# Kernel tuning notes

Hardware: AMD Instinct MI355X
Metric: run time of the kernel (lower is better)

Reference implementation:

```python
import jax, jax.numpy as jnp
import numpy as np

N_NODES = 100000
N_EDGES = 1600000
N_GRAPHS = 256


def gcn_conv(x, src, dst, edge_weight, W, b, num_nodes):
    """PyG GCNConv: add self-loops, symmetric degree normalization,
    linear transform, scatter-add aggregation, bias."""
    loop = jnp.arange(num_nodes)
    s = jnp.concatenate([src, loop])
    d = jnp.concatenate([dst, loop])
    ew = jnp.concatenate([edge_weight, jnp.ones((num_nodes,), dtype=edge_weight.dtype)])
    deg = jax.ops.segment_sum(ew, d, num_segments=num_nodes)  # [N]
    dinv = jnp.where(deg > 0, deg ** -0.5, 0.0)
    norm = dinv[s] * ew * dinv[d]  # [E+N]
    h = x @ W  # [N, out]
    msg = h[s] * norm[:, None]  # gather + scale
    out = jax.ops.segment_sum(msg, d, num_segments=num_nodes)  # scatter-add
    return out + b


def global_mean_pool(x, batch, num_graphs):
    s = jax.ops.segment_sum(x, batch, num_segments=num_graphs)
    cnt = jax.ops.segment_sum(jnp.ones((x.shape[0],), dtype=x.dtype), batch, num_segments=num_graphs)
    return s / jnp.maximum(cnt, 1.0)[:, None]


def setup_inputs() -> dict:
    key = jax.random.key(0)
    ks = jax.random.split(key, 12)
    x = jax.random.normal(ks[0], (N_NODES, 128), dtype=jnp.float32)
    edge_index = jax.random.randint(ks[1], (2, N_EDGES), 0, N_NODES, dtype=jnp.int64)
    edge_attr = jax.random.uniform(ks[2], (N_EDGES,), dtype=jnp.float32)
    batch = jnp.sort(jax.random.randint(ks[3], (N_NODES,), 0, N_GRAPHS, dtype=jnp.int64))
    def lin(k, fan_in, fan_out):
        lim = 1.0 / np.sqrt(fan_in)
        kw, kb = jax.random.split(k)
        W = jax.random.uniform(kw, (fan_in, fan_out), minval=-lim, maxval=lim, dtype=jnp.float32)
        b = jax.random.uniform(kb, (fan_out,), minval=-lim, maxval=lim, dtype=jnp.float32)
        return W, b
    W1, b1 = lin(ks[4], 128, 64)
    W2, b2 = lin(ks[5], 64, 64)
    W3, b3 = lin(ks[6], 64, 64)
    Wl, bl = lin(ks[7], 64, 10)
    return {"x": x, "edge_index": edge_index, "edge_attr": edge_attr, "batch": batch,
            "W1": W1, "b1": b1, "W2": W2, "b2": b2, "W3": W3, "b3": b3, "Wl": Wl, "bl": bl}


def reference(x, edge_index, edge_attr, batch, W1, b1, W2, b2, W3, b3, Wl, bl):
    src, dst = edge_index[0], edge_index[1]
    n = x.shape[0]
    h = jax.nn.relu(gcn_conv(x, src, dst, edge_attr, W1, b1, n))
    h = jax.nn.relu(gcn_conv(h, src, dst, edge_attr, W2, b2, n))
    h = jax.nn.relu(gcn_conv(h, src, dst, edge_attr, W3, b3, n))
    g = global_mean_pool(h, batch, N_GRAPHS)  # [G, 64]
    return g @ Wl + bl  # [G, num_classes]
```

## Files before the change

kernel.cpp:

```cpp
#include <hip/hip_runtime.h>
#include <hip/hip_bf16.h>

#define N_NODES  100000
#define N_EDGES  1600000
#define N_GRAPHS 256
#define F 64
#define NBUCK  782
#define CHUNK  4096
#define NCHUNK 391


__global__ __launch_bounds__(1024) void k_hist(const int* __restrict__ dst, int* __restrict__ hist) {
    __shared__ int lh[NBUCK];
    int tid = threadIdx.x, chunk = blockIdx.x;
    for (int j = tid; j < NBUCK; j += 1024) lh[j] = 0;
    __syncthreads();
    int e0 = chunk * CHUNK;
#pragma unroll
    for (int i = 0; i < CHUNK / 1024; i++) {
        int e = e0 + i * 1024 + tid;
        if (e < N_EDGES) atomicAdd(&lh[dst[e] >> 7], 1);
    }
    __syncthreads();
    for (int j = tid; j < NBUCK; j += 1024) hist[chunk * NBUCK + j] = lh[j];
}

__global__ __launch_bounds__(512) void k_colscan(int* __restrict__ hist, int* __restrict__ btot) {
    __shared__ int ts[512];
    int b = blockIdx.x, tid = threadIdx.x;
    int v = (tid < NCHUNK) ? hist[tid * NBUCK + b] : 0;
    ts[tid] = v;
    __syncthreads();
    int x = v;
    for (int off = 1; off < 512; off <<= 1) {
        int t = (tid >= off) ? ts[tid - off] : 0;
        __syncthreads();
        x += t; ts[tid] = x;
        __syncthreads();
    }
    if (tid < NCHUNK) hist[tid * NBUCK + b] = x - v;
    if (tid == 511) btot[b] = x;
}

__global__ __launch_bounds__(512) void k_bscan_gstart(const int* __restrict__ btot, int* __restrict__ base,
                                                      const int* __restrict__ batch, int* __restrict__ gstart) {
    if (blockIdx.x == 1) {
        int g = threadIdx.x;
        if (g > N_GRAPHS) return;
        int lo = 0, hi = N_NODES;
        while (lo < hi) {
            int mid = (lo + hi) >> 1;
            if (batch[mid] < g) lo = mid + 1; else hi = mid;
        }
        gstart[g] = lo;
        return;
    }
    __shared__ int ts[256];
    int tid = threadIdx.x;
    int v[4], loc[4], run = 0;
    if (tid < 256) {
#pragma unroll
        for (int k = 0; k < 4; k++) {
            int c = tid * 4 + k;
            v[k] = (c < NBUCK) ? btot[c] : 0;
            loc[k] = run; run += v[k];
        }
        ts[tid] = run;
    }
    __syncthreads();
    int x = run;
    for (int off = 1; off < 256; off <<= 1) {
        int t = (tid >= off && tid < 256) ? ts[tid - off] : 0;
        __syncthreads();
        if (tid < 256) { x += t; ts[tid] = x; }
        __syncthreads();
    }
    if (tid < 256) {
        int texcl = x - run;
#pragma unroll
        for (int k = 0; k < 4; k++) {
            int c = tid * 4 + k;
            if (c < NBUCK) base[c] = texcl + loc[k];
        }
        if (tid == 255) base[NBUCK] = x;
    }
}

__global__ __launch_bounds__(1024) void k_partition(const int* __restrict__ src, const int* __restrict__ dst,
                                                    const float* __restrict__ ew,
                                                    const int* __restrict__ hist, const int* __restrict__ base,
                                                    long long* __restrict__ part) {
    __shared__ int cursor[NBUCK];
    int tid = threadIdx.x, chunk = blockIdx.x;
    for (int j = tid; j < NBUCK; j += 1024) cursor[j] = base[j] + hist[chunk * NBUCK + j];
    __syncthreads();
    int e0 = chunk * CHUNK;
#pragma unroll
    for (int i = 0; i < CHUNK / 1024; i++) {
        int e = e0 + i * 1024 + tid;
        if (e < N_EDGES) {
            int d = dst[e];
            int pos = atomicAdd(&cursor[d >> 7], 1);
            unsigned lo = (unsigned)src[e] | ((unsigned)(d & 127) << 17);
            long long rec = (long long)((unsigned long long)lo |
                            ((unsigned long long)__float_as_uint(ew[e]) << 32));
            part[pos] = rec;
        }
    }
}

__global__ __launch_bounds__(512) void k_deg(const long long* __restrict__ part,
                                             const int* __restrict__ base,
                                             float* __restrict__ dinv_g, int* __restrict__ row_off) {
    __shared__ float fdeg[128];
    __shared__ int   cnt[128];
    __shared__ int   sc[128];
    int b = blockIdx.x, tid = threadIdx.x;
    if (tid < 128) { fdeg[tid] = 1.0f; cnt[tid] = 0; }
    __syncthreads();
    int e0 = base[b], e1 = base[b + 1];
    for (int k = e0 + tid; k < e1; k += 512) {
        long long rec = part[k];
        int d7 = ((int)rec >> 17) & 127;
        atomicAdd(&fdeg[d7], __uint_as_float((unsigned)(rec >> 32)));
        atomicAdd(&cnt[d7], 1);
    }
    __syncthreads();
    int myc = 0, x = 0;
    if (tid < 128) {
        int node = b * 128 + tid;
        if (node < N_NODES) dinv_g[node] = rsqrtf(fdeg[tid]);
        myc = cnt[tid]; x = myc; sc[tid] = x;
    }
    __syncthreads();
    for (int off = 1; off < 128; off <<= 1) {
        int t = (tid < 128 && tid >= off) ? sc[tid - off] : 0;
        __syncthreads();
        if (tid < 128) { x += t; sc[tid] = x; }
        __syncthreads();
    }
    if (tid < 128) {
        int node = b * 128 + tid;
        if (node < N_NODES) row_off[node] = e0 + (x - myc);
    }
    if (b == 0 && tid == 0) row_off[N_NODES] = N_EDGES;
}

__global__ __launch_bounds__(512) void k_scat(const long long* __restrict__ part,
                                              const int* __restrict__ base,
                                              const float* __restrict__ dinv_g,
                                              const int* __restrict__ row_off,
                                              int2* __restrict__ esec) {
    __shared__ int   cursor[128];
    __shared__ float sdinv[128];
    int b = blockIdx.x, tid = threadIdx.x;
    if (tid < 128) {
        int node = b * 128 + tid;
        cursor[tid] = row_off[node < N_NODES ? node : N_NODES];
        sdinv[tid]  = dinv_g[node < N_NODES ? node : 0];
    }
    __syncthreads();
    int e0 = base[b], e1 = base[b + 1];
    for (int k = e0 + tid; k < e1; k += 512) {
        long long rec = part[k];
        int lo = (int)rec;
        int d7 = (lo >> 17) & 127;
        int s  = lo & 0x1FFFF;
        float w = __uint_as_float((unsigned)(rec >> 32));
        float coef = (w * sdinv[d7]) * dinv_g[s];
        int pos = atomicAdd(&cursor[d7], 1);
        esec[pos] = make_int2(s << 7, __float_as_int(coef));
    }
    if (b == 0 && tid < 16) esec[N_EDGES + tid] = make_int2(0, 0);
}

template <int K, bool BF16IN>
__global__ __launch_bounds__(256) void k_gemm(const void* __restrict__ Xv,
                                              const float* __restrict__ W,
                                              __hip_bfloat16* __restrict__ H) {
    constexpr int KC = 32;
    constexpr int XP = KC + 4;
    __shared__ float Xs[256 * XP];
    __shared__ float Ws[KC * F];
    const int tid  = threadIdx.x;
    const int fgrp = tid & 7;
    const int ngrp = tid >> 3;
    const int f0   = fgrp * 8;
    const int nb   = blockIdx.x * 256;

    float acc[8][8];
#pragma unroll
    for (int i = 0; i < 8; i++)
#pragma unroll
        for (int j = 0; j < 8; j++) acc[i][j] = 0.0f;

    for (int kc = 0; kc < K; kc += KC) {
        if (kc) __syncthreads();
        if (BF16IN) {
            const unsigned short* X = (const unsigned short*)Xv;
#pragma unroll
            for (int pass = 0; pass < 4; pass++) {
                int idx = tid + pass * 256;
                int r = idx >> 2, q = idx & 3;
                int gr = nb + r; if (gr >= N_NODES) gr = N_NODES - 1;
                uint4 v = *(const uint4*)&X[(size_t)gr * K + kc + q * 8];
                float* dp = &Xs[r * XP + q * 8];
                dp[0] = __uint_as_float(v.x << 16);
                dp[1] = __uint_as_float(v.x & 0xffff0000u);
                dp[2] = __uint_as_float(v.y << 16);
                dp[3] = __uint_as_float(v.y & 0xffff0000u);
                dp[4] = __uint_as_float(v.z << 16);
                dp[5] = __uint_as_float(v.z & 0xffff0000u);
                dp[6] = __uint_as_float(v.w << 16);
                dp[7] = __uint_as_float(v.w & 0xffff0000u);
            }
        } else {
            const float* X = (const float*)Xv;
#pragma unroll
            for (int pass = 0; pass < 8; pass++) {
                int idx = tid + pass * 256;
                int r = idx >> 3, q = idx & 7;
                int gr = nb + r; if (gr >= N_NODES) gr = N_NODES - 1;
                float4 v = *(const float4*)&X[(size_t)gr * K + kc + q * 4];
                *(float4*)&Xs[r * XP + q * 4] = v;
            }
        }
#pragma unroll
        for (int pass = 0; pass < 2; pass++) {
            int idx = tid + pass * 256;
            float4 v = *(const float4*)&W[(size_t)(kc + (idx >> 4)) * F + (idx & 15) * 4];
            *(float4*)&Ws[idx * 4] = v;
        }
        __syncthreads();
#pragma unroll
        for (int k = 0; k < KC; k += 4) {
            float4 wa[4], wb[4];
#pragma unroll
            for (int kk = 0; kk < 4; kk++) {
                wa[kk] = *(const float4*)&Ws[(k + kk) * F + f0];
                wb[kk] = *(const float4*)&Ws[(k + kk) * F + f0 + 4];
            }
#pragma unroll
            for (int i = 0; i < 8; i++) {
                float4 xv = *(const float4*)&Xs[(ngrp + 32 * i) * XP + k];
#pragma unroll
                for (int kk = 0; kk < 4; kk++) {
                    float xk = (kk == 0) ? xv.x : (kk == 1) ? xv.y : (kk == 2) ? xv.z : xv.w;
                    acc[i][0] = fmaf(xk, wa[kk].x, acc[i][0]);
                    acc[i][1] = fmaf(xk, wa[kk].y, acc[i][1]);
                    acc[i][2] = fmaf(xk, wa[kk].z, acc[i][2]);
                    acc[i][3] = fmaf(xk, wa[kk].w, acc[i][3]);
                    acc[i][4] = fmaf(xk, wb[kk].x, acc[i][4]);
                    acc[i][5] = fmaf(xk, wb[kk].y, acc[i][5]);
                    acc[i][6] = fmaf(xk, wb[kk].z, acc[i][6]);
                    acc[i][7] = fmaf(xk, wb[kk].w, acc[i][7]);
                }
            }
        }
    }
#pragma unroll
    for (int i = 0; i < 8; i++) {
        int gn = nb + ngrp + 32 * i;
        if (gn < N_NODES) {
            __hip_bfloat16 hb[8];
#pragma unroll
            for (int j = 0; j < 8; j++) hb[j] = __float2bfloat16(acc[i][j]);
            *(uint4*)&H[(size_t)gn * F + f0] = *(uint4*)hb;
        }
    }
}

__global__ __launch_bounds__(256) void k_agg(const __hip_bfloat16* __restrict__ H,
                                             const int* __restrict__ row_off,
                                             const int2* __restrict__ esec,
                                             const float* __restrict__ dinv,
                                             const float* __restrict__ bias,
                                             __hip_bfloat16* __restrict__ O) {
    int wv   = threadIdx.x >> 6;
    int lane = threadIdx.x & 63;
    int np   = blockIdx.x * 16 + wv * 4;
    int q  = lane >> 3;
    int f8 = lane & 7;
    int r0 = __builtin_amdgcn_readfirstlane(row_off[np]);
    int r1 = __builtin_amdgcn_readfirstlane(row_off[np + 1]);
    int r2 = __builtin_amdgcn_readfirstlane(row_off[np + 2]);
    int r3 = __builtin_amdgcn_readfirstlane(row_off[np + 3]);
    int r4 = __builtin_amdgcn_readfirstlane(row_off[np + 4]);
    const char* Hbase = (const char*)H;

    float a0[8], a1[8], a2[8], a3[8];
#pragma unroll
    for (int u = 0; u < 8; u++) { a0[u] = 0.0f; a1[u] = 0.0f; a2[u] = 0.0f; a3[u] = 0.0f; }

    int l0 = r1 - r0, l1 = r2 - r1, l2 = r3 - r2, l3 = r4 - r3;
    int ml = l0 > l1 ? l0 : l1;
    if (l2 > ml) ml = l2;
    if (l3 > ml) ml = l3;
    int iters = (ml + 7) >> 3;
    int j0 = r0 + q, j1 = r1 + q, j2 = r2 + q, j3 = r3 + q;
    for (int it = 0; it < iters; it++, j0 += 8, j1 += 8, j2 += 8, j3 += 8) {
        int i0 = j0 < N_EDGES ? j0 : N_EDGES;
        int i1 = j1 < N_EDGES ? j1 : N_EDGES;
        int i2 = j2 < N_EDGES ? j2 : N_EDGES;
        int i3 = j3 < N_EDGES ? j3 : N_EDGES;
        int2 ev0 = esec[i0];
        int2 ev1 = esec[i1];
        int2 ev2 = esec[i2];
        int2 ev3 = esec[i3];
        float c0 = (j0 < r1) ? __int_as_float(ev0.y) : 0.0f;
        float c1 = (j1 < r2) ? __int_as_float(ev1.y) : 0.0f;
        float c2 = (j2 < r3) ? __int_as_float(ev2.y) : 0.0f;
        float c3 = (j3 < r4) ? __int_as_float(ev3.y) : 0.0f;
        uint4 h0 = *(const uint4*)(Hbase + (unsigned)ev0.x + (f8 << 4));
        uint4 h1 = *(const uint4*)(Hbase + (unsigned)ev1.x + (f8 << 4));
        uint4 h2 = *(const uint4*)(Hbase + (unsigned)ev2.x + (f8 << 4));
        uint4 h3 = *(const uint4*)(Hbase + (unsigned)ev3.x + (f8 << 4));
        a0[0] = fmaf(c0, __uint_as_float(h0.x << 16),         a0[0]);
        a0[1] = fmaf(c0, __uint_as_float(h0.x & 0xffff0000u), a0[1]);
        a0[2] = fmaf(c0, __uint_as_float(h0.y << 16),         a0[2]);
        a0[3] = fmaf(c0, __uint_as_float(h0.y & 0xffff0000u), a0[3]);
        a0[4] = fmaf(c0, __uint_as_float(h0.z << 16),         a0[4]);
        a0[5] = fmaf(c0, __uint_as_float(h0.z & 0xffff0000u), a0[5]);
        a0[6] = fmaf(c0, __uint_as_float(h0.w << 16),         a0[6]);
        a0[7] = fmaf(c0, __uint_as_float(h0.w & 0xffff0000u), a0[7]);
        a1[0] = fmaf(c1, __uint_as_float(h1.x << 16),         a1[0]);
        a1[1] = fmaf(c1, __uint_as_float(h1.x & 0xffff0000u), a1[1]);
        a1[2] = fmaf(c1, __uint_as_float(h1.y << 16),         a1[2]);
        a1[3] = fmaf(c1, __uint_as_float(h1.y & 0xffff0000u), a1[3]);
        a1[4] = fmaf(c1, __uint_as_float(h1.z << 16),         a1[4]);
        a1[5] = fmaf(c1, __uint_as_float(h1.z & 0xffff0000u), a1[5]);
        a1[6] = fmaf(c1, __uint_as_float(h1.w << 16),         a1[6]);
        a1[7] = fmaf(c1, __uint_as_float(h1.w & 0xffff0000u), a1[7]);
        a2[0] = fmaf(c2, __uint_as_float(h2.x << 16),         a2[0]);
        a2[1] = fmaf(c2, __uint_as_float(h2.x & 0xffff0000u), a2[1]);
        a2[2] = fmaf(c2, __uint_as_float(h2.y << 16),         a2[2]);
        a2[3] = fmaf(c2, __uint_as_float(h2.y & 0xffff0000u), a2[3]);
        a2[4] = fmaf(c2, __uint_as_float(h2.z << 16),         a2[4]);
        a2[5] = fmaf(c2, __uint_as_float(h2.z & 0xffff0000u), a2[5]);
        a2[6] = fmaf(c2, __uint_as_float(h2.w << 16),         a2[6]);
        a2[7] = fmaf(c2, __uint_as_float(h2.w & 0xffff0000u), a2[7]);
        a3[0] = fmaf(c3, __uint_as_float(h3.x << 16),         a3[0]);
        a3[1] = fmaf(c3, __uint_as_float(h3.x & 0xffff0000u), a3[1]);
        a3[2] = fmaf(c3, __uint_as_float(h3.y << 16),         a3[2]);
        a3[3] = fmaf(c3, __uint_as_float(h3.y & 0xffff0000u), a3[3]);
        a3[4] = fmaf(c3, __uint_as_float(h3.z << 16),         a3[4]);
        a3[5] = fmaf(c3, __uint_as_float(h3.z & 0xffff0000u), a3[5]);
        a3[6] = fmaf(c3, __uint_as_float(h3.w << 16),         a3[6]);
        a3[7] = fmaf(c3, __uint_as_float(h3.w & 0xffff0000u), a3[7]);
    }
#pragma unroll
    for (int m = 8; m < 64; m <<= 1) {
#pragma unroll
        for (int u = 0; u < 8; u++) {
            a0[u] += __shfl_xor(a0[u], m);
            a1[u] += __shfl_xor(a1[u], m);
            a2[u] += __shfl_xor(a2[u], m);
            a3[u] += __shfl_xor(a3[u], m);
        }
    }
    if (q < 4) {
        int node = np + q;
        float av[8];
#pragma unroll
        for (int u = 0; u < 8; u++) {
            float t01 = (q & 1) ? a1[u] : a0[u];
            float t23 = (q & 1) ? a3[u] : a2[u];
            av[u] = (q & 2) ? t23 : t01;
        }
        float di = dinv[node];
        float di2 = di * di;
        uint4 hs = *(const uint4*)(Hbase + (size_t)node * 128 + (f8 << 4));
        float hv[8];
        hv[0] = __uint_as_float(hs.x << 16);
        hv[1] = __uint_as_float(hs.x & 0xffff0000u);
        hv[2] = __uint_as_float(hs.y << 16);
        hv[3] = __uint_as_float(hs.y & 0xffff0000u);
        hv[4] = __uint_as_float(hs.z << 16);
        hv[5] = __uint_as_float(hs.z & 0xffff0000u);
        hv[6] = __uint_as_float(hs.w << 16);
        hv[7] = __uint_as_float(hs.w & 0xffff0000u);
        const float4* bp = (const float4*)(bias + f8 * 8);
        float4 bv0 = bp[0], bv1 = bp[1];
        float r[8];
        r[0] = fmaxf(av[0] + bv0.x + di2 * hv[0], 0.0f);
        r[1] = fmaxf(av[1] + bv0.y + di2 * hv[1], 0.0f);
        r[2] = fmaxf(av[2] + bv0.z + di2 * hv[2], 0.0f);
        r[3] = fmaxf(av[3] + bv0.w + di2 * hv[3], 0.0f);
        r[4] = fmaxf(av[4] + bv1.x + di2 * hv[4], 0.0f);
        r[5] = fmaxf(av[5] + bv1.y + di2 * hv[5], 0.0f);
        r[6] = fmaxf(av[6] + bv1.z + di2 * hv[6], 0.0f);
        r[7] = fmaxf(av[7] + bv1.w + di2 * hv[7], 0.0f);
        __hip_bfloat16 hb[8];
#pragma unroll
        for (int u = 0; u < 8; u++) hb[u] = __float2bfloat16(r[u]);
        *(uint4*)&O[(size_t)node * F + f8 * 8] = *(uint4*)hb;
    }
}

__global__ __launch_bounds__(256) void k_pool_linear(const __hip_bfloat16* __restrict__ H,
                                                     const int* __restrict__ gstart,
                                                     const float* __restrict__ Wl,
                                                     const float* __restrict__ bl,
                                                     float* __restrict__ out) {
    int g = blockIdx.x;
    int beg = gstart[g], end = gstart[g + 1];
    int lane = threadIdx.x & 63, wv = threadIdx.x >> 6;
    float acc = 0.0f;
    for (int r = beg + wv; r < end; r += 4)
        acc += __bfloat162float(H[(size_t)r * F + lane]);
    __shared__ float s[4][F];
    s[wv][lane] = acc;
    __syncthreads();
    if (wv == 0) {
        float tot = s[0][lane] + s[1][lane] + s[2][lane] + s[3][lane];
        float cntf = (float)(end - beg);
        float p = tot / fmaxf(cntf, 1.0f);
        for (int c = 0; c < 10; c++) {
            float v = p * Wl[lane * 10 + c];
            for (int off = 32; off; off >>= 1) v += __shfl_down(v, off);
            if (lane == 0) out[g * 10 + c] = v + bl[c];
        }
    }
}


extern "C" void kernel_launch(void* const* d_in, const int* in_sizes, int n_in,
                              void* d_out, int out_size, void* d_ws, size_t ws_size,
                              hipStream_t stream) {
    const float* x    = (const float*)d_in[0];
    const int*   ei   = (const int*)d_in[1];
    const float* ea   = (const float*)d_in[2];
    const int*   bat  = (const int*)d_in[3];
    const float* W1   = (const float*)d_in[4];
    const float* b1   = (const float*)d_in[5];
    const float* W2   = (const float*)d_in[6];
    const float* b2   = (const float*)d_in[7];
    const float* W3   = (const float*)d_in[8];
    const float* b3   = (const float*)d_in[9];
    const float* Wl   = (const float*)d_in[10];
    const float* bl   = (const float*)d_in[11];
    float* out = (float*)d_out;

    const int* src = ei;
    const int* dst = ei + N_EDGES;

    char* ws = (char*)d_ws;
    size_t off = 0;
    auto carve = [&](size_t bytes) {
        void* p = ws + off;
        off += (bytes + 255) & ~(size_t)255;
        return p;
    };
    float*          dinv    = (float*)carve(N_NODES * 4);
    int*            row_off = (int*)  carve((N_NODES + 1) * 4);
    int2*           esec    = (int2*) carve(((size_t)N_EDGES + 16) * 8);
    __hip_bfloat16* hbuf    = (__hip_bfloat16*)carve((size_t)N_NODES * F * 2);
    __hip_bfloat16* obuf    = (__hip_bfloat16*)carve((size_t)N_NODES * F * 4);
    int*            gstart  = (int*)  carve((N_GRAPHS + 1) * 4);
    (void)ws_size; (void)in_sizes; (void)n_in; (void)out_size;

    long long* part = (long long*)hbuf;
    char* alias = (char*)obuf + (size_t)N_NODES * F * 2;
    int* hist = (int*)alias;                         alias += (size_t)NCHUNK * NBUCK * 4;
    int* btot = (int*)alias;                         alias += (NBUCK + 8) * 4;
    int* base = (int*)alias;

    const int GB = (N_NODES + 255) / 256;

    k_hist        <<<NCHUNK, 1024, 0, stream>>>(dst, hist);
    k_colscan     <<<NBUCK,  512,  0, stream>>>(hist, btot);
    k_bscan_gstart<<<2,      512,  0, stream>>>(btot, base, bat, gstart);
    k_partition   <<<NCHUNK, 1024, 0, stream>>>(src, dst, ea, hist, base, part);
    k_deg         <<<NBUCK,  512,  0, stream>>>(part, base, dinv, row_off);
    k_scat        <<<NBUCK,  512,  0, stream>>>(part, base, dinv, row_off, esec);

    k_gemm<128, false><<<GB, 256, 0, stream>>>(x, W1, hbuf);
    k_agg<<<N_NODES / 16, 256, 0, stream>>>(hbuf, row_off, esec, dinv, b1, obuf);
    k_gemm<64, true><<<GB, 256, 0, stream>>>(obuf, W2, hbuf);
    k_agg<<<N_NODES / 16, 256, 0, stream>>>(hbuf, row_off, esec, dinv, b2, obuf);
    k_gemm<64, true><<<GB, 256, 0, stream>>>(obuf, W3, hbuf);
    k_agg<<<N_NODES / 16, 256, 0, stream>>>(hbuf, row_off, esec, dinv, b3, obuf);

    k_pool_linear<<<N_GRAPHS, 256, 0, stream>>>(obuf, gstart, Wl, bl, out);
}
```

Before: 382.1 us.

## Fuse edge partition with first GEMM and double per-iteration gathers in aggregation

Merges the edge-partition kernel and the first-layer GEMM into one launch whose blocks split between the two independent jobs. The partition output moves to its own workspace buffer instead of aliasing hbuf, which is what allows the GEMM to run concurrently with it and saves a launch. The aggregation loop now issues 8 edge/feature gathers per iteration instead of 4, giving more loads in flight at the cost of extra registers. The tail padding of esec grows to 32 entries to match, and the partition blocks drop from 1024 to 256 threads.

```diff
diff --git a/kernel.cpp b/kernel.cpp
--- a/kernel.cpp
+++ b/kernel.cpp
@@ -8,6 +8,7 @@
 #define NBUCK  782
 #define CHUNK  4096
 #define NCHUNK 391
+#define GB     391
 
 
 __global__ __launch_bounds__(1024) void k_hist(const int* __restrict__ dst, int* __restrict__ hist) {
@@ -86,25 +87,101 @@
     }
 }
 
-__global__ __launch_bounds__(1024) void k_partition(const int* __restrict__ src, const int* __restrict__ dst,
-                                                    const float* __restrict__ ew,
-                                                    const int* __restrict__ hist, const int* __restrict__ base,
-                                                    long long* __restrict__ part) {
-    __shared__ int cursor[NBUCK];
-    int tid = threadIdx.x, chunk = blockIdx.x;
-    for (int j = tid; j < NBUCK; j += 1024) cursor[j] = base[j] + hist[chunk * NBUCK + j];
-    __syncthreads();
-    int e0 = chunk * CHUNK;
-#pragma unroll
-    for (int i = 0; i < CHUNK / 1024; i++) {
-        int e = e0 + i * 1024 + tid;
-        if (e < N_EDGES) {
-            int d = dst[e];
-            int pos = atomicAdd(&cursor[d >> 7], 1);
-            unsigned lo = (unsigned)src[e] | ((unsigned)(d & 127) << 17);
-            long long rec = (long long)((unsigned long long)lo |
-                            ((unsigned long long)__float_as_uint(ew[e]) << 32));
-            part[pos] = rec;
+__global__ __launch_bounds__(256) void k_part_gemm1(
+    const int* __restrict__ src, const int* __restrict__ dst, const float* __restrict__ ew,
+    const int* __restrict__ hist, const int* __restrict__ base, long long* __restrict__ part,
+    const float* __restrict__ X, const float* __restrict__ W, __hip_bfloat16* __restrict__ H) {
+    constexpr int KC = 32;
+    constexpr int XP = KC + 4;
+    __shared__ float smem[256 * XP + KC * F];
+    const int tid = threadIdx.x;
+
+    if (blockIdx.x < NCHUNK) {
+        int* cursor = (int*)smem;
+        int chunk = blockIdx.x;
+        for (int j = tid; j < NBUCK; j += 256) cursor[j] = base[j] + hist[chunk * NBUCK + j];
+        __syncthreads();
+        int e0 = chunk * CHUNK;
+#pragma unroll
+        for (int i = 0; i < CHUNK / 256; i++) {
+            int e = e0 + i * 256 + tid;
+            if (e < N_EDGES) {
+                int d = dst[e];
+                int pos = atomicAdd(&cursor[d >> 7], 1);
+                unsigned lo = (unsigned)src[e] | ((unsigned)(d & 127) << 17);
+                long long rec = (long long)((unsigned long long)lo |
+                                ((unsigned long long)__float_as_uint(ew[e]) << 32));
+                part[pos] = rec;
+            }
+        }
+        return;
+    }
+
+    float* Xs = smem;
+    float* Ws = smem + 256 * XP;
+    const int fgrp = tid & 7;
+    const int ngrp = tid >> 3;
+    const int f0   = fgrp * 8;
+    const int nb   = (blockIdx.x - NCHUNK) * 256;
+    constexpr int K = 128;
+
+    float acc[8][8];
+#pragma unroll
+    for (int i = 0; i < 8; i++)
+#pragma unroll
+        for (int j = 0; j < 8; j++) acc[i][j] = 0.0f;
+
+    for (int kc = 0; kc < K; kc += KC) {
+        if (kc) __syncthreads();
+#pragma unroll
+        for (int pass = 0; pass < 8; pass++) {
+            int idx = tid + pass * 256;
+            int r = idx >> 3, q = idx & 7;
+            int gr = nb + r; if (gr >= N_NODES) gr = N_NODES - 1;
+            float4 v = *(const float4*)&X[(size_t)gr * K + kc + q * 4];
+            *(float4*)&Xs[r * XP + q * 4] = v;
+        }
+#pragma unroll
+        for (int pass = 0; pass < 2; pass++) {
+            int idx = tid + pass * 256;
+            float4 v = *(const float4*)&W[(size_t)(kc + (idx >> 4)) * F + (idx & 15) * 4];
+            *(float4*)&Ws[idx * 4] = v;
+        }
+        __syncthreads();
+#pragma unroll
+        for (int k = 0; k < KC; k += 4) {
+            float4 wa[4], wb[4];
+#pragma unroll
+            for (int kk = 0; kk < 4; kk++) {
+                wa[kk] = *(const float4*)&Ws[(k + kk) * F + f0];
+                wb[kk] = *(const float4*)&Ws[(k + kk) * F + f0 + 4];
+            }
+#pragma unroll
+            for (int i = 0; i < 8; i++) {
+                float4 xv = *(const float4*)&Xs[(ngrp + 32 * i) * XP + k];
+#pragma unroll
+                for (int kk = 0; kk < 4; kk++) {
+                    float xk = (kk == 0) ? xv.x : (kk == 1) ? xv.y : (kk == 2) ? xv.z : xv.w;
+                    acc[i][0] = fmaf(xk, wa[kk].x, acc[i][0]);
+                    acc[i][1] = fmaf(xk, wa[kk].y, acc[i][1]);
+                    acc[i][2] = fmaf(xk, wa[kk].z, acc[i][2]);
+                    acc[i][3] = fmaf(xk, wa[kk].w, acc[i][3]);
+                    acc[i][4] = fmaf(xk, wb[kk].x, acc[i][4]);
+                    acc[i][5] = fmaf(xk, wb[kk].y, acc[i][5]);
+                    acc[i][6] = fmaf(xk, wb[kk].z, acc[i][6]);
+                    acc[i][7] = fmaf(xk, wb[kk].w, acc[i][7]);
+                }
+            }
+        }
+    }
+#pragma unroll
+    for (int i = 0; i < 8; i++) {
+        int gn = nb + ngrp + 32 * i;
+        if (gn < N_NODES) {
+            __hip_bfloat16 hb[8];
+#pragma unroll
+            for (int j = 0; j < 8; j++) hb[j] = __float2bfloat16(acc[i][j]);
+            *(uint4*)&H[(size_t)gn * F + f0] = *(uint4*)hb;
         }
     }
 }
@@ -171,11 +248,11 @@
         int pos = atomicAdd(&cursor[d7], 1);
         esec[pos] = make_int2(s << 7, __float_as_int(coef));
     }
-    if (b == 0 && tid < 16) esec[N_EDGES + tid] = make_int2(0, 0);
-}
-
-template <int K, bool BF16IN>
-__global__ __launch_bounds__(256) void k_gemm(const void* __restrict__ Xv,
+    if (b == 0 && tid < 32) esec[N_EDGES + tid] = make_int2(0, 0);
+}
+
+template <int K>
+__global__ __launch_bounds__(256) void k_gemm(const unsigned short* __restrict__ X,
                                               const float* __restrict__ W,
                                               __hip_bfloat16* __restrict__ H) {
     constexpr int KC = 32;
@@ -196,34 +273,21 @@
 
     for (int kc = 0; kc < K; kc += KC) {
         if (kc) __syncthreads();
-        if (BF16IN) {
-            const unsigned short* X = (const unsigned short*)Xv;
-#pragma unroll
-            for (int pass = 0; pass < 4; pass++) {
-                int idx = tid + pass * 256;
-                int r = idx >> 2, q = idx & 3;
-                int gr = nb + r; if (gr >= N_NODES) gr = N_NODES - 1;
-                uint4 v = *(const uint4*)&X[(size_t)gr * K + kc + q * 8];
-                float* dp = &Xs[r * XP + q * 8];
-                dp[0] = __uint_as_float(v.x << 16);
-                dp[1] = __uint_as_float(v.x & 0xffff0000u);
-                dp[2] = __uint_as_float(v.y << 16);
-                dp[3] = __uint_as_float(v.y & 0xffff0000u);
-                dp[4] = __uint_as_float(v.z << 16);
-                dp[5] = __uint_as_float(v.z & 0xffff0000u);
-                dp[6] = __uint_as_float(v.w << 16);
-                dp[7] = __uint_as_float(v.w & 0xffff0000u);
-            }
-        } else {
-            const float* X = (const float*)Xv;
-#pragma unroll
-            for (int pass = 0; pass < 8; pass++) {
-                int idx = tid + pass * 256;
-                int r = idx >> 3, q = idx & 7;
-                int gr = nb + r; if (gr >= N_NODES) gr = N_NODES - 1;
-                float4 v = *(const float4*)&X[(size_t)gr * K + kc + q * 4];
-                *(float4*)&Xs[r * XP + q * 4] = v;
-            }
+#pragma unroll
+        for (int pass = 0; pass < 4; pass++) {
+            int idx = tid + pass * 256;
+            int r = idx >> 2, q = idx & 3;
+            int gr = nb + r; if (gr >= N_NODES) gr = N_NODES - 1;
+            uint4 v = *(const uint4*)&X[(size_t)gr * K + kc + q * 8];
+            float* dp = &Xs[r * XP + q * 8];
+            dp[0] = __uint_as_float(v.x << 16);
+            dp[1] = __uint_as_float(v.x & 0xffff0000u);
+            dp[2] = __uint_as_float(v.y << 16);
+            dp[3] = __uint_as_float(v.y & 0xffff0000u);
+            dp[4] = __uint_as_float(v.z << 16);
+            dp[5] = __uint_as_float(v.z & 0xffff0000u);
+            dp[6] = __uint_as_float(v.w << 16);
+            dp[7] = __uint_as_float(v.w & 0xffff0000u);
         }
 #pragma unroll
         for (int pass = 0; pass < 2; pass++) {
@@ -288,83 +352,63 @@
     int r4 = __builtin_amdgcn_readfirstlane(row_off[np + 4]);
     const char* Hbase = (const char*)H;
 
-    float a0[8], a1[8], a2[8], a3[8];
-#pragma unroll
-    for (int u = 0; u < 8; u++) { a0[u] = 0.0f; a1[u] = 0.0f; a2[u] = 0.0f; a3[u] = 0.0f; }
-
+    float a[4][8];
+#pragma unroll
+    for (int n = 0; n < 4; n++)
+#pragma unroll
+        for (int u = 0; u < 8; u++) a[n][u] = 0.0f;
+
+    int jb[4] = { r0 + q, r1 + q, r2 + q, r3 + q };
+    int re[4] = { r1, r2, r3, r4 };
     int l0 = r1 - r0, l1 = r2 - r1, l2 = r3 - r2, l3 = r4 - r3;
     int ml = l0 > l1 ? l0 : l1;
     if (l2 > ml) ml = l2;
     if (l3 > ml) ml = l3;
-    int iters = (ml + 7) >> 3;
-    int j0 = r0 + q, j1 = r1 + q, j2 = r2 + q, j3 = r3 + q;
-    for (int it = 0; it < iters; it++, j0 += 8, j1 += 8, j2 += 8, j3 += 8) {
-        int i0 = j0 < N_EDGES ? j0 : N_EDGES;
-        int i1 = j1 < N_EDGES ? j1 : N_EDGES;
-        int i2 = j2 < N_EDGES ? j2 : N_EDGES;
-        int i3 = j3 < N_EDGES ? j3 : N_EDGES;
-        int2 ev0 = esec[i0];
-        int2 ev1 = esec[i1];
-        int2 ev2 = esec[i2];
-        int2 ev3 = esec[i3];
-        float c0 = (j0 < r1) ? __int_as_float(ev0.y) : 0.0f;
-        float c1 = (j1 < r2) ? __int_as_float(ev1.y) : 0.0f;
-        float c2 = (j2 < r3) ? __int_as_float(ev2.y) : 0.0f;
-        float c3 = (j3 < r4) ? __int_as_float(ev3.y) : 0.0f;
-        uint4 h0 = *(const uint4*)(Hbase + (unsigned)ev0.x + (f8 << 4));
-        uint4 h1 = *(const uint4*)(Hbase + (unsigned)ev1.x + (f8 << 4));
-        uint4 h2 = *(const uint4*)(Hbase + (unsigned)ev2.x + (f8 << 4));
-        uint4 h3 = *(const uint4*)(Hbase + (unsigned)ev3.x + (f8 << 4));
-        a0[0] = fmaf(c0, __uint_as_float(h0.x << 16),         a0[0]);
-        a0[1] = fmaf(c0, __uint_as_float(h0.x & 0xffff0000u), a0[1]);
-        a0[2] = fmaf(c0, __uint_as_float(h0.y << 16),         a0[2]);
-        a0[3] = fmaf(c0, __uint_as_float(h0.y & 0xffff0000u), a0[3]);
-        a0[4] = fmaf(c0, __uint_as_float(h0.z << 16),         a0[4]);
-        a0[5] = fmaf(c0, __uint_as_float(h0.z & 0xffff0000u), a0[5]);
-        a0[6] = fmaf(c0, __uint_as_float(h0.w << 16),         a0[6]);
-        a0[7] = fmaf(c0, __uint_as_float(h0.w & 0xffff0000u), a0[7]);
-        a1[0] = fmaf(c1, __uint_as_float(h1.x << 16),         a1[0]);
-        a1[1] = fmaf(c1, __uint_as_float(h1.x & 0xffff0000u), a1[1]);
-        a1[2] = fmaf(c1, __uint_as_float(h1.y << 16),         a1[2]);
-        a1[3] = fmaf(c1, __uint_as_float(h1.y & 0xffff0000u), a1[3]);
-        a1[4] = fmaf(c1, __uint_as_float(h1.z << 16),         a1[4]);
-        a1[5] = fmaf(c1, __uint_as_float(h1.z & 0xffff0000u), a1[5]);
-        a1[6] = fmaf(c1, __uint_as_float(h1.w << 16),         a1[6]);
-        a1[7] = fmaf(c1, __uint_as_float(h1.w & 0xffff0000u), a1[7]);
-        a2[0] = fmaf(c2, __uint_as_float(h2.x << 16),         a2[0]);
-        a2[1] = fmaf(c2, __uint_as_float(h2.x & 0xffff0000u), a2[1]);
-        a2[2] = fmaf(c2, __uint_as_float(h2.y << 16),         a2[2]);
-        a2[3] = fmaf(c2, __uint_as_float(h2.y & 0xffff0000u), a2[3]);
-        a2[4] = fmaf(c2, __uint_as_float(h2.z << 16),         a2[4]);
-        a2[5] = fmaf(c2, __uint_as_float(h2.z & 0xffff0000u), a2[5]);
-        a2[6] = fmaf(c2, __uint_as_float(h2.w << 16),         a2[6]);
-        a2[7] = fmaf(c2, __uint_as_float(h2.w & 0xffff0000u), a2[7]);
-        a3[0] = fmaf(c3, __uint_as_float(h3.x << 16),         a3[0]);
-        a3[1] = fmaf(c3, __uint_as_float(h3.x & 0xffff0000u), a3[1]);
-        a3[2] = fmaf(c3, __uint_as_float(h3.y << 16),         a3[2]);
-        a3[3] = fmaf(c3, __uint_as_float(h3.y & 0xffff0000u), a3[3]);
-        a3[4] = fmaf(c3, __uint_as_float(h3.z << 16),         a3[4]);
-        a3[5] = fmaf(c3, __uint_as_float(h3.z & 0xffff0000u), a3[5]);
-        a3[6] = fmaf(c3, __uint_as_float(h3.w << 16),         a3[6]);
-        a3[7] = fmaf(c3, __uint_as_float(h3.w & 0xffff0000u), a3[7]);
+    int iters = (ml + 15) >> 4;
+
+    for (int it = 0; it < iters; it++) {
+        int2 ev[8];
+#pragma unroll
+        for (int s = 0; s < 8; s++) {
+            int jj = jb[s >> 1] + ((s & 1) << 3);
+            int ii = jj < N_EDGES ? jj : N_EDGES;
+            ev[s] = esec[ii];
+        }
+        uint4 h[8];
+#pragma unroll
+        for (int s = 0; s < 8; s++)
+            h[s] = *(const uint4*)(Hbase + (unsigned)ev[s].x + (f8 << 4));
+#pragma unroll
+        for (int s = 0; s < 8; s++) {
+            int n = s >> 1;
+            int jj = jb[n] + ((s & 1) << 3);
+            float c = (jj < re[n]) ? __int_as_float(ev[s].y) : 0.0f;
+            a[n][0] = fmaf(c, __uint_as_float(h[s].x << 16),         a[n][0]);
+            a[n][1] = fmaf(c, __uint_as_float(h[s].x & 0xffff0000u), a[n][1]);
+            a[n][2] = fmaf(c, __uint_as_float(h[s].y << 16),         a[n][2]);
+            a[n][3] = fmaf(c, __uint_as_float(h[s].y & 0xffff0000u), a[n][3]);
+            a[n][4] = fmaf(c, __uint_as_float(h[s].z << 16),         a[n][4]);
+            a[n][5] = fmaf(c, __uint_as_float(h[s].z & 0xffff0000u), a[n][5]);
+            a[n][6] = fmaf(c, __uint_as_float(h[s].w << 16),         a[n][6]);
+            a[n][7] = fmaf(c, __uint_as_float(h[s].w & 0xffff0000u), a[n][7]);
+        }
+#pragma unroll
+        for (int n = 0; n < 4; n++) jb[n] += 16;
     }
 #pragma unroll
     for (int m = 8; m < 64; m <<= 1) {
 #pragma unroll
-        for (int u = 0; u < 8; u++) {
-            a0[u] += __shfl_xor(a0[u], m);
-            a1[u] += __shfl_xor(a1[u], m);
-            a2[u] += __shfl_xor(a2[u], m);
-            a3[u] += __shfl_xor(a3[u], m);
-        }
+        for (int n = 0; n < 4; n++)
+#pragma unroll
+            for (int u = 0; u < 8; u++) a[n][u] += __shfl_xor(a[n][u], m);
     }
     if (q < 4) {
         int node = np + q;
         float av[8];
 #pragma unroll
         for (int u = 0; u < 8; u++) {
-            float t01 = (q & 1) ? a1[u] : a0[u];
-            float t23 = (q & 1) ? a3[u] : a2[u];
+            float t01 = (q & 1) ? a[1][u] : a[0][u];
+            float t23 = (q & 1) ? a[3][u] : a[2][u];
             av[u] = (q & 2) ? t23 : t01;
         }
         float di = dinv[node];
@@ -453,32 +497,28 @@
     };
     float*          dinv    = (float*)carve(N_NODES * 4);
     int*            row_off = (int*)  carve((N_NODES + 1) * 4);
-    int2*           esec    = (int2*) carve(((size_t)N_EDGES + 16) * 8);
+    int2*           esec    = (int2*) carve(((size_t)N_EDGES + 32) * 8);
     __hip_bfloat16* hbuf    = (__hip_bfloat16*)carve((size_t)N_NODES * F * 2);
-    __hip_bfloat16* obuf    = (__hip_bfloat16*)carve((size_t)N_NODES * F * 4);
+    __hip_bfloat16* obuf    = (__hip_bfloat16*)carve((size_t)N_NODES * F * 2);
+    long long*      part    = (long long*)carve((size_t)N_EDGES * 8);
+    int*            hist    = (int*)  carve((size_t)NCHUNK * NBUCK * 4);
+    int*            btot    = (int*)  carve((NBUCK + 8) * 4);
+    int*            base    = (int*)  carve((NBUCK + 8) * 4);
     int*            gstart  = (int*)  carve((N_GRAPHS + 1) * 4);
     (void)ws_size; (void)in_sizes; (void)n_in; (void)out_size;
 
-    long long* part = (long long*)hbuf;
-    char* alias = (char*)obuf + (size_t)N_NODES * F * 2;
-    int* hist = (int*)alias;                         alias += (size_t)NCHUNK * NBUCK * 4;
-    int* btot = (int*)alias;                         alias += (NBUCK + 8) * 4;
-    int* base = (int*)alias;
-
-    const int GB = (N_NODES + 255) / 256;
-
-    k_hist        <<<NCHUNK, 1024, 0, stream>>>(dst, hist);
-    k_colscan     <<<NBUCK,  512,  0, stream>>>(hist, btot);
-    k_bscan_gstart<<<2,      512,  0, stream>>>(btot, base, bat, gstart);
-    k_partition   <<<NCHUNK, 1024, 0, stream>>>(src, dst, ea, hist, base, part);
-    k_deg         <<<NBUCK,  512,  0, stream>>>(part, base, dinv, row_off);
-    k_scat        <<<NBUCK,  512,  0, stream>>>(part, base, dinv, row_off, esec);
-
-    k_gemm<128, false><<<GB, 256, 0, stream>>>(x, W1, hbuf);
+    k_hist        <<<NCHUNK,      1024, 0, stream>>>(dst, hist);
+    k_colscan     <<<NBUCK,       512,  0, stream>>>(hist, btot);
+    k_bscan_gstart<<<2,           512,  0, stream>>>(btot, base, bat, gstart);
+    k_part_gemm1  <<<NCHUNK + GB, 256,  0, stream>>>(src, dst, ea, hist, base, part,
+                                                     x, W1, hbuf);
+    k_deg         <<<NBUCK,       512,  0, stream>>>(part, base, dinv, row_off);
+    k_scat        <<<NBUCK,       512,  0, stream>>>(part, base, dinv, row_off, esec);
+
     k_agg<<<N_NODES / 16, 256, 0, stream>>>(hbuf, row_off, esec, dinv, b1, obuf);
-    k_gemm<64, true><<<GB, 256, 0, stream>>>(obuf, W2, hbuf);
+    k_gemm<64><<<GB, 256, 0, stream>>>((const unsigned short*)obuf, W2, hbuf);
     k_agg<<<N_NODES / 16, 256, 0, stream>>>(hbuf, row_off, esec, dinv, b2, obuf);
-    k_gemm<64, true><<<GB, 256, 0, stream>>>(obuf, W3, hbuf);
+    k_gemm<64><<<GB, 256, 0, stream>>>((const unsigned short*)obuf, W3, hbuf);
     k_agg<<<N_NODES / 16, 256, 0, stream>>>(hbuf, row_off, esec, dinv, b3, obuf);
 
     k_pool_linear<<<N_GRAPHS, 256, 0, stream>>>(obuf, gstart, Wl, bl, out);
```

Measured after the change: 599.3 us. 1.57x slower.
